# Optimization experiments

Measured on AMD Instinct MI355X. Metric: run time of the kernel, lower is better.

## Reference

```python
import jax, jax.numpy as jnp
import numpy as np

N_NODES = 50000
N_EDGES = 800000
IN_DIM = 128
HIDDEN = 128
N_GRAPHS = 512


def setup_inputs() -> dict:
    key = jax.random.key(0)
    ks = jax.random.split(key, 9)
    x = jax.random.normal(ks[0], (N_NODES, IN_DIM), dtype=jnp.float32)
    edge_index = jax.random.randint(ks[1], (2, N_EDGES), 0, N_NODES, dtype=jnp.int32)
    batch = jnp.sort(jax.random.randint(ks[2], (N_NODES,), 0, N_GRAPHS, dtype=jnp.int32))
    # GCNConv params: linear (no bias) applied before propagation, bias added after.
    s1 = 1.0 / np.sqrt(IN_DIM)
    s2 = 1.0 / np.sqrt(HIDDEN)
    W1 = jax.random.uniform(ks[3], (IN_DIM, HIDDEN), jnp.float32, -s1, s1)
    b1 = jnp.zeros((HIDDEN,), jnp.float32)
    W2 = jax.random.uniform(ks[4], (HIDDEN, HIDDEN), jnp.float32, -s2, s2)
    b2 = jnp.zeros((HIDDEN,), jnp.float32)
    Wl = jax.random.uniform(ks[5], (HIDDEN, 1), jnp.float32, -s2, s2)
    bl = jax.random.uniform(ks[6], (1,), jnp.float32, -s2, s2)
    return {"x": x, "edge_index": edge_index, "batch": batch,
            "W1": W1, "b1": b1, "W2": W2, "b2": b2, "Wl": Wl, "bl": bl}


def gcn_conv(x, W, b, src, dst):
    # PyG GCNConv: h = D^{-1/2} (A + I) D^{-1/2} (x W) + b, with self-loops.
    h = x @ W                                        # [N, H]
    deg = jnp.zeros((N_NODES,), h.dtype).at[dst].add(1.0) + 1.0  # +1 for self-loop
    dinv = jax.lax.rsqrt(deg)                        # [N]
    msg = h[src] * (dinv[src] * dinv[dst])[:, None]  # [E, H] gather + normalize
    agg = jax.ops.segment_sum(msg, dst, num_segments=N_NODES)    # scatter-add
    agg = agg + h * (dinv * dinv)[:, None]           # self-loop contribution
    return agg + b


def reference(x, edge_index, batch, W1, b1, W2, b2, Wl, bl):
    src, dst = edge_index[0], edge_index[1]
    h = jax.nn.relu(gcn_conv(x, W1, b1, src, dst))
    h = jax.nn.relu(gcn_conv(h, W2, b2, src, dst))
    # global mean pool over graphs
    sums = jax.ops.segment_sum(h, batch, num_segments=N_GRAPHS)  # [G, H]
    cnt = jax.ops.segment_sum(jnp.ones((N_NODES,), h.dtype), batch, num_segments=N_GRAPHS)
    pooled = sums / jnp.maximum(cnt, 1.0)[:, None]
    return pooled @ Wl + bl
```

## Files before the change

### kernel.cpp

```cpp
#include <hip/hip_runtime.h>
#include <hip/hip_bf16.h>

#define N_NODES 50000
#define N_EDGES 800000
#define DIM 128
#define N_GRAPHS 512
#define NBUCK ((N_NODES + 63) / 64)
#define SC_CH 2048
#define SCT_BLOCKS ((N_EDGES + SC_CH - 1) / SC_CH)
#define GEMM_BLOCKS 782

typedef unsigned int uint;
typedef unsigned short ushort;
typedef __attribute__((ext_vector_type(8))) short short8;
typedef __attribute__((ext_vector_type(4))) float f32x4;

__device__ __forceinline__ ushort f2bf(float f) {
    uint u = __float_as_uint(f);
    uint r = (u + 0x7FFF + ((u >> 16) & 1)) >> 16;
    return (ushort)r;
}
__device__ __forceinline__ uint pack2(float a, float b) {
    return (uint)f2bf(a) | ((uint)f2bf(b) << 16);
}
__device__ __forceinline__ float2 unpack2(uint v) {
    return make_float2(__uint_as_float(v << 16), __uint_as_float(v & 0xFFFF0000u));
}


__global__ __launch_bounds__(256) void k_init(const float* __restrict__ W1,
                                              const float* __restrict__ W2,
                                              uint* __restrict__ wf1,
                                              uint* __restrict__ wf2,
                                              int* __restrict__ bucketCnt) {
    int t = blockIdx.x * 256 + threadIdx.x;
    if (t < NBUCK) bucketCnt[t] = 0;
    const float* W = (t < 8192) ? W1 : W2;
    uint* dst = (t < 8192) ? wf1 : wf2;
    int r = t & 8191;
    int j2 = r & 3;
    int lane = (r >> 2) & 63;
    int tk = r >> 8;
    int kc = tk & 3, ct = tk >> 2;
    int j = j2 * 2;
    int k = kc * 32 + (lane >> 4) * 8 + j;
    int n = ct * 16 + (lane & 15);
    dst[r] = pack2(W[k * 128 + n], W[(k + 1) * 128 + n]);
}


__global__ __launch_bounds__(1024) void k_bcount(const int* __restrict__ ei,
                                                 int* __restrict__ bucketCnt, int E) {
    __shared__ int h[NBUCK];
    int tid = threadIdx.x;
    for (int t = tid; t < NBUCK; t += 1024) h[t] = 0;
    __syncthreads();
    for (int e = blockIdx.x * 1024 + tid; e < E; e += gridDim.x * 1024)
        atomicAdd(&h[ei[E + e] >> 6], 1);
    __syncthreads();
    for (int t = tid; t < NBUCK; t += 1024) {
        int c = h[t];
        if (c) atomicAdd(&bucketCnt[t], c);
    }
}


__global__ __launch_bounds__(256) void k_bscan(const int* __restrict__ bucketCnt,
                                               int* __restrict__ bucketStart,
                                               int* __restrict__ bucketCursor) {
    __shared__ int wsum4[4];
    int tid = threadIdx.x;
    int base = tid * 4;
    int v[4];
    #pragma unroll
    for (int i = 0; i < 4; ++i)
        v[i] = (base + i < NBUCK) ? bucketCnt[base + i] : 0;
    int tot = v[0] + v[1] + v[2] + v[3];
    int lane = tid & 63, w = tid >> 6;
    int sc = tot;
    #pragma unroll
    for (int off = 1; off < 64; off <<= 1) {
        int u = __shfl_up(sc, off, 64);
        if (lane >= off) sc += u;
    }
    if (lane == 63) wsum4[w] = sc;
    __syncthreads();
    int woff = 0;
    #pragma unroll
    for (int ww = 0; ww < 4; ++ww) woff += (ww < w) ? wsum4[ww] : 0;
    int run = woff + sc - tot;
    #pragma unroll
    for (int i = 0; i < 4; ++i) {
        if (base + i < NBUCK) {
            bucketStart[base + i] = run;
            bucketCursor[base + i] = run;
        }
        run += v[i];
    }
    if (tid == 255) bucketStart[NBUCK] = run;
}


template<bool BF16IN, bool SCALE>
__device__ __forceinline__ void gemm_body(int blk, const void* __restrict__ Xv,
                                          const uint* __restrict__ Wfrag,
                                          const float* __restrict__ dinv,
                                          uint* __restrict__ out, int N) {
    int wv = threadIdx.x >> 6, lane = threadIdx.x & 63;
    int strip = blk * 4 + wv;
    int row0 = strip * 16;
    if (row0 >= N) return;
    int m = lane & 15;
    int kg = lane >> 4;
    int arow = row0 + m;
    bool valid = arow < N;

    short8 af[4];
    if constexpr (!BF16IN) {
        const float* X = (const float*)Xv;
        const float* base = X + (size_t)arow * DIM + kg * 8;
        #pragma unroll
        for (int kc = 0; kc < 4; ++kc) {
            float4 a0 = make_float4(0.f, 0.f, 0.f, 0.f), a1 = a0;
            if (valid) {
                a0 = *(const float4*)(base + kc * 32);
                a1 = *(const float4*)(base + kc * 32 + 4);
            }
            short8 f;
            f[0] = (short)f2bf(a0.x); f[1] = (short)f2bf(a0.y);
            f[2] = (short)f2bf(a0.z); f[3] = (short)f2bf(a0.w);
            f[4] = (short)f2bf(a1.x); f[5] = (short)f2bf(a1.y);
            f[6] = (short)f2bf(a1.z); f[7] = (short)f2bf(a1.w);
            af[kc] = f;
        }
    } else {
        const uint* X = (const uint*)Xv;
        const uint* base = X + (size_t)arow * 64 + kg * 4;
        #pragma unroll
        for (int kc = 0; kc < 4; ++kc) {
            union { uint4 u; short8 s; } cv;
            cv.u = valid ? *(const uint4*)(base + kc * 16) : make_uint4(0, 0, 0, 0);
            af[kc] = cv.s;
        }
    }

    f32x4 acc[8];
    #pragma unroll
    for (int ct = 0; ct < 8; ++ct) acc[ct] = (f32x4){0.f, 0.f, 0.f, 0.f};

    #pragma unroll
    for (int ct = 0; ct < 8; ++ct) {
        #pragma unroll
        for (int kc = 0; kc < 4; ++kc) {
            union { uint4 u; short8 s; } bv;
            bv.u = *(const uint4*)(Wfrag + ((size_t)(ct * 4 + kc) * 64 + lane) * 4);
            acc[ct] = __builtin_amdgcn_mfma_f32_16x16x32_bf16(af[kc], bv.s, acc[ct], 0, 0, 0);
        }
    }

    ushort* ob = (ushort*)out;
    #pragma unroll
    for (int reg = 0; reg < 4; ++reg) {
        int orow = row0 + kg * 4 + reg;
        if (orow < N) {
            float di = SCALE ? dinv[orow] : 1.0f;
            size_t rb = (size_t)orow * DIM + m;
            #pragma unroll
            for (int ct = 0; ct < 8; ++ct)
                ob[rb + ct * 16] = f2bf(SCALE ? acc[ct][reg] * di : acc[ct][reg]);
        }
    }
}


__global__ __launch_bounds__(256) void k_mega1(const int* __restrict__ ei,
                                               int* __restrict__ bucketCursor,
                                               uint* __restrict__ epk,
                                               const float* __restrict__ x,
                                               const uint* __restrict__ wf1,
                                               uint* __restrict__ hs) {
    __shared__ int hc[NBUCK];
    __shared__ int hbase[NBUCK];
    if (blockIdx.x >= SCT_BLOCKS) {
        gemm_body<false, false>(blockIdx.x - SCT_BLOCKS, x, wf1, nullptr, hs, N_NODES);
        return;
    }
    int tid = threadIdx.x;
    int e0 = blockIdx.x * SC_CH;
    int e1 = min(e0 + SC_CH, N_EDGES);
    for (int t = tid; t < NBUCK; t += 256) hc[t] = 0;
    __syncthreads();
    for (int e = e0 + tid; e < e1; e += 256)
        atomicAdd(&hc[ei[N_EDGES + e] >> 6], 1);
    __syncthreads();
    for (int t = tid; t < NBUCK; t += 256) {
        int c = hc[t];
        hbase[t] = c ? atomicAdd(&bucketCursor[t], c) : 0;
        hc[t] = 0;
    }
    __syncthreads();
    for (int e = e0 + tid; e < e1; e += 256) {
        int s = ei[e], d = ei[N_EDGES + e];
        int b = d >> 6;
        int off = atomicAdd(&hc[b], 1);
        epk[hbase[b] + off] = (uint)s | ((uint)(d & 63) << 16);
    }
}


__global__ __launch_bounds__(256) void k_localcsr(const uint* __restrict__ epk,
                                                  const int* __restrict__ bucketStart,
                                                  int* __restrict__ rowStart,
                                                  float* __restrict__ dinv,
                                                  int* __restrict__ csr) {
    __shared__ int cnt[64];
    __shared__ int cur[64];
    int tid = threadIdx.x;
    int b = blockIdx.x;
    int b0 = b << 6;
    int s = bucketStart[b], e = bucketStart[b + 1];
    if (tid < 64) cnt[tid] = 0;
    __syncthreads();
    for (int i = s + tid; i < e; i += 256)
        atomicAdd(&cnt[(epk[i] >> 16) & 63], 1);
    __syncthreads();
    if (tid < 64) {
        int c = cnt[tid];
        int sc = c;
        #pragma unroll
        for (int off = 1; off < 64; off <<= 1) {
            int u = __shfl_up(sc, off, 64);
            if (tid >= off) sc += u;
        }
        int excl = sc - c;
        int node = b0 + tid;
        if (node < N_NODES) {
            rowStart[node] = s + excl;
            dinv[node] = rsqrtf((float)c + 1.0f);
        }
        cur[tid] = s + excl;
    }
    if (tid == 0 && b == NBUCK - 1) rowStart[N_NODES] = e;
    __syncthreads();
    for (int i = s + tid; i < e; i += 256) {
        uint p = epk[i];
        int pos = atomicAdd(&cur[(p >> 16) & 63], 1);
        csr[pos] = (int)(p & 0xFFFFu);
    }
}


__global__ __launch_bounds__(256) void k_lin2(const uint* __restrict__ Xb,
                                              const uint* __restrict__ Wfrag,
                                              const float* __restrict__ dinv,
                                              uint* __restrict__ out, int N) {
    gemm_body<true, true>(blockIdx.x, Xb, Wfrag, dinv, out, N);
}


template<bool FUSE_HEAD, bool SCALE_SRC>
__global__ __launch_bounds__(256) void k_aggregate(const uint* __restrict__ HS,
                                                   const int* __restrict__ rowStart,
                                                   const int* __restrict__ csr,
                                                   const float* __restrict__ dinv,
                                                   const float* __restrict__ bias,
                                                   const float* __restrict__ Wl,
                                                   uint* __restrict__ outRow,
                                                   float* __restrict__ outY, int n) {
    int wv = threadIdx.x >> 6, lane = threadIdx.x & 63;
    int nid = blockIdx.x * 4 + wv;
    if (nid >= n) return;
    float di = dinv[nid];
    float2 acc = unpack2(HS[(size_t)nid * 64 + lane]);
    if constexpr (SCALE_SRC) { acc.x *= di; acc.y *= di; }
    int beg = rowStart[nid], end = rowStart[nid + 1];
    int e = beg;
    for (; e + 7 < end; e += 8) {
        int s0 = csr[e],     s1 = csr[e + 1], s2 = csr[e + 2], s3 = csr[e + 3];
        int s4 = csr[e + 4], s5 = csr[e + 5], s6 = csr[e + 6], s7 = csr[e + 7];
        float2 f0 = unpack2(HS[(size_t)s0 * 64 + lane]);
        float2 f1 = unpack2(HS[(size_t)s1 * 64 + lane]);
        float2 f2 = unpack2(HS[(size_t)s2 * 64 + lane]);
        float2 f3 = unpack2(HS[(size_t)s3 * 64 + lane]);
        float2 f4 = unpack2(HS[(size_t)s4 * 64 + lane]);
        float2 f5 = unpack2(HS[(size_t)s5 * 64 + lane]);
        float2 f6 = unpack2(HS[(size_t)s6 * 64 + lane]);
        float2 f7 = unpack2(HS[(size_t)s7 * 64 + lane]);
        if constexpr (SCALE_SRC) {
            float d0 = dinv[s0], d1 = dinv[s1], d2 = dinv[s2], d3 = dinv[s3];
            float d4 = dinv[s4], d5 = dinv[s5], d6 = dinv[s6], d7 = dinv[s7];
            acc.x += ((f0.x * d0 + f1.x * d1) + (f2.x * d2 + f3.x * d3))
                   + ((f4.x * d4 + f5.x * d5) + (f6.x * d6 + f7.x * d7));
            acc.y += ((f0.y * d0 + f1.y * d1) + (f2.y * d2 + f3.y * d3))
                   + ((f4.y * d4 + f5.y * d5) + (f6.y * d6 + f7.y * d7));
        } else {
            acc.x += ((f0.x + f1.x) + (f2.x + f3.x)) + ((f4.x + f5.x) + (f6.x + f7.x));
            acc.y += ((f0.y + f1.y) + (f2.y + f3.y)) + ((f4.y + f5.y) + (f6.y + f7.y));
        }
    }
    if (e + 3 < end) {
        int s0 = csr[e], s1 = csr[e + 1], s2 = csr[e + 2], s3 = csr[e + 3];
        float2 f0 = unpack2(HS[(size_t)s0 * 64 + lane]);
        float2 f1 = unpack2(HS[(size_t)s1 * 64 + lane]);
        float2 f2 = unpack2(HS[(size_t)s2 * 64 + lane]);
        float2 f3 = unpack2(HS[(size_t)s3 * 64 + lane]);
        if constexpr (SCALE_SRC) {
            float d0 = dinv[s0], d1 = dinv[s1], d2 = dinv[s2], d3 = dinv[s3];
            acc.x += (f0.x * d0 + f1.x * d1) + (f2.x * d2 + f3.x * d3);
            acc.y += (f0.y * d0 + f1.y * d1) + (f2.y * d2 + f3.y * d3);
        } else {
            acc.x += (f0.x + f1.x) + (f2.x + f3.x);
            acc.y += (f0.y + f1.y) + (f2.y + f3.y);
        }
        e += 4;
    }
    if (e + 1 < end) {
        int s0 = csr[e], s1 = csr[e + 1];
        float2 f0 = unpack2(HS[(size_t)s0 * 64 + lane]);
        float2 f1 = unpack2(HS[(size_t)s1 * 64 + lane]);
        if constexpr (SCALE_SRC) {
            float d0 = dinv[s0], d1 = dinv[s1];
            acc.x += f0.x * d0 + f1.x * d1;
            acc.y += f0.y * d0 + f1.y * d1;
        } else {
            acc.x += f0.x + f1.x;
            acc.y += f0.y + f1.y;
        }
        e += 2;
    }
    if (e < end) {
        int s0 = csr[e];
        float2 f0 = unpack2(HS[(size_t)s0 * 64 + lane]);
        if constexpr (SCALE_SRC) {
            float d0 = dinv[s0];
            acc.x += f0.x * d0;
            acc.y += f0.y * d0;
        } else {
            acc.x += f0.x;
            acc.y += f0.y;
        }
    }
    int c = lane * 2;
    float ox = fmaxf(acc.x * di + bias[c], 0.f);
    float oy = fmaxf(acc.y * di + bias[c + 1], 0.f);
    if constexpr (!FUSE_HEAD) {
        outRow[(size_t)nid * 64 + lane] = pack2(ox, oy);
    } else {
        float part = ox * Wl[c] + oy * Wl[c + 1];
        #pragma unroll
        for (int off = 32; off > 0; off >>= 1) part += __shfl_down(part, off, 64);
        if (lane == 0) outY[nid] = part;
    }
}


__global__ __launch_bounds__(64) void k_pool_y(const float* __restrict__ y,
                                               const int* __restrict__ batch,
                                               const float* __restrict__ bl,
                                               float* __restrict__ out, int n) {
    int g = blockIdx.x;
    int lane = threadIdx.x;
    int lo = 0, hi = n;
    while (lo < hi) { int mid = (lo + hi) >> 1; if (batch[mid] < g) lo = mid + 1; else hi = mid; }
    int s = lo;
    hi = n;
    while (lo < hi) { int mid = (lo + hi) >> 1; if (batch[mid] < g + 1) lo = mid + 1; else hi = mid; }
    int e = lo;

    float sum = 0.f;
    for (int i = s + lane; i < e; i += 64) sum += y[i];
    #pragma unroll
    for (int off = 32; off > 0; off >>= 1) sum += __shfl_down(sum, off, 64);
    if (lane == 0) out[g] = sum / fmaxf((float)(e - s), 1.0f) + bl[0];
}


extern "C" void kernel_launch(void* const* d_in, const int* in_sizes, int n_in,
                              void* d_out, int out_size, void* d_ws, size_t ws_size,
                              hipStream_t stream) {
    const float* x  = (const float*)d_in[0];
    const int*   ei = (const int*)d_in[1];
    const int*   batch = (const int*)d_in[2];
    const float* W1 = (const float*)d_in[3];
    const float* b1 = (const float*)d_in[4];
    const float* W2 = (const float*)d_in[5];
    const float* b2 = (const float*)d_in[6];
    const float* Wl = (const float*)d_in[7];
    const float* bl = (const float*)d_in[8];
    float* out = (float*)d_out;

    uint* hs  = (uint*)d_ws;
    uint* h2b = hs + (size_t)N_NODES * 64;
    float* dinv = (float*)(h2b + (size_t)N_NODES * 64);
    float* ynode = dinv + N_NODES;
    int* rowStart = (int*)(ynode + N_NODES);
    int* bucketCnt = rowStart + N_NODES + 4;
    int* bucketStart = bucketCnt + 788;
    int* bucketCursor = bucketStart + 788;
    int* csr = bucketCursor + 788;
    uint* epk = (uint*)(csr + N_EDGES);
    uint* wf1 = epk + N_EDGES;
    uint* wf2 = wf1 + 8192;

    k_init<<<64, 256, 0, stream>>>(W1, W2, wf1, wf2, bucketCnt);

    k_bcount<<<64, 1024, 0, stream>>>(ei, bucketCnt, N_EDGES);

    k_bscan<<<1, 256, 0, stream>>>(bucketCnt, bucketStart, bucketCursor);

    k_mega1<<<SCT_BLOCKS + GEMM_BLOCKS, 256, 0, stream>>>(ei, bucketCursor, epk, x, wf1, hs);

    k_localcsr<<<NBUCK, 256, 0, stream>>>(epk, bucketStart, rowStart, dinv, csr);

    int aggGrid = (N_NODES + 3) / 4;

    k_aggregate<false, true><<<aggGrid, 256, 0, stream>>>(
        hs, rowStart, csr, dinv, b1, Wl, h2b, ynode, N_NODES);

    k_lin2<<<GEMM_BLOCKS, 256, 0, stream>>>(h2b, wf2, dinv, hs, N_NODES);

    k_aggregate<true, false><<<aggGrid, 256, 0, stream>>>(
        hs, rowStart, csr, dinv, b2, Wl, h2b, ynode, N_NODES);

    k_pool_y<<<N_GRAPHS, 64, 0, stream>>>(ynode, batch, bl, out, N_NODES);
}
```

Baseline: 142.3 us.

## Fuse CSR build stages into one persistent kernel with grid barriers

Replaces the separate bucket-count, scan, scatter and local-CSR kernels with a single kernel. 512 CSR blocks synchronise through a software grid barrier (atomic counter plus generation flag), while extra blocks in the same launch run the first GEMM. The aim is to remove several kernel launch gaps and the per-stage drain. The barrier only works if all 512 CSR blocks are resident at once, so there is a deadlock risk, and the spin-waiting blocks compete with the GEMM blocks for compute units.

```diff
diff --git a/kernel.cpp b/kernel.cpp
--- a/kernel.cpp
+++ b/kernel.cpp
@@ -6,8 +6,8 @@
 #define DIM 128
 #define N_GRAPHS 512
 #define NBUCK ((N_NODES + 63) / 64)
-#define SC_CH 2048
-#define SCT_BLOCKS ((N_EDGES + SC_CH - 1) / SC_CH)
+#define CSRB 512
+#define EPB ((N_EDGES + CSRB - 1) / CSRB)
 #define GEMM_BLOCKS 782
 
 typedef unsigned int uint;
@@ -32,9 +32,11 @@
                                               const float* __restrict__ W2,
                                               uint* __restrict__ wf1,
                                               uint* __restrict__ wf2,
-                                              int* __restrict__ bucketCnt) {
+                                              int* __restrict__ bucketCnt,
+                                              int* __restrict__ bar) {
     int t = blockIdx.x * 256 + threadIdx.x;
     if (t < NBUCK) bucketCnt[t] = 0;
+    if (t >= NBUCK && t < NBUCK + 2) bar[t - NBUCK] = 0;
     const float* W = (t < 8192) ? W1 : W2;
     uint* dst = (t < 8192) ? wf1 : wf2;
     int r = t & 8191;
@@ -49,55 +51,22 @@
 }
 
 
-__global__ __launch_bounds__(1024) void k_bcount(const int* __restrict__ ei,
-                                                 int* __restrict__ bucketCnt, int E) {
-    __shared__ int h[NBUCK];
-    int tid = threadIdx.x;
-    for (int t = tid; t < NBUCK; t += 1024) h[t] = 0;
+__device__ __forceinline__ void gbar(int* barCnt, int* barGen, int phase) {
     __syncthreads();
-    for (int e = blockIdx.x * 1024 + tid; e < E; e += gridDim.x * 1024)
-        atomicAdd(&h[ei[E + e] >> 6], 1);
+    if (threadIdx.x == 0) {
+        __threadfence();
+        if (atomicAdd(barCnt, 1) == CSRB - 1) {
+            atomicExch(barCnt, 0);
+            __threadfence();
+            atomicAdd(barGen, 1);
+        } else {
+            while (atomicAdd(barGen, 0) <= phase) {
+                __builtin_amdgcn_s_sleep(2);
+            }
+        }
+        __threadfence();
+    }
     __syncthreads();
-    for (int t = tid; t < NBUCK; t += 1024) {
-        int c = h[t];
-        if (c) atomicAdd(&bucketCnt[t], c);
-    }
-}
-
-
-__global__ __launch_bounds__(256) void k_bscan(const int* __restrict__ bucketCnt,
-                                               int* __restrict__ bucketStart,
-                                               int* __restrict__ bucketCursor) {
-    __shared__ int wsum4[4];
-    int tid = threadIdx.x;
-    int base = tid * 4;
-    int v[4];
-    #pragma unroll
-    for (int i = 0; i < 4; ++i)
-        v[i] = (base + i < NBUCK) ? bucketCnt[base + i] : 0;
-    int tot = v[0] + v[1] + v[2] + v[3];
-    int lane = tid & 63, w = tid >> 6;
-    int sc = tot;
-    #pragma unroll
-    for (int off = 1; off < 64; off <<= 1) {
-        int u = __shfl_up(sc, off, 64);
-        if (lane >= off) sc += u;
-    }
-    if (lane == 63) wsum4[w] = sc;
-    __syncthreads();
-    int woff = 0;
-    #pragma unroll
-    for (int ww = 0; ww < 4; ++ww) woff += (ww < w) ? wsum4[ww] : 0;
-    int run = woff + sc - tot;
-    #pragma unroll
-    for (int i = 0; i < 4; ++i) {
-        if (base + i < NBUCK) {
-            bucketStart[base + i] = run;
-            bucketCursor[base + i] = run;
-        }
-        run += v[i];
-    }
-    if (tid == 255) bucketStart[NBUCK] = run;
 }
 
 
@@ -173,21 +142,33 @@
 }
 
 
-__global__ __launch_bounds__(256) void k_mega1(const int* __restrict__ ei,
+__global__ __launch_bounds__(256) void k_build(const int* __restrict__ ei,
+                                               int* __restrict__ bucketCnt,
+                                               int* __restrict__ bucketStart,
                                                int* __restrict__ bucketCursor,
                                                uint* __restrict__ epk,
+                                               int* __restrict__ rowStart,
+                                               float* __restrict__ dinv,
+                                               int* __restrict__ csr,
+                                               int* __restrict__ bar,
                                                const float* __restrict__ x,
                                                const uint* __restrict__ wf1,
                                                uint* __restrict__ hs) {
+    if (blockIdx.x >= CSRB) {
+        gemm_body<false, false>(blockIdx.x - CSRB, x, wf1, nullptr, hs, N_NODES);
+        return;
+    }
     __shared__ int hc[NBUCK];
     __shared__ int hbase[NBUCK];
-    if (blockIdx.x >= SCT_BLOCKS) {
-        gemm_body<false, false>(blockIdx.x - SCT_BLOCKS, x, wf1, nullptr, hs, N_NODES);
-        return;
-    }
+    __shared__ int wsum4[4];
+    __shared__ int cnt[64];
+    __shared__ int cur[64];
+    int cb = blockIdx.x;
     int tid = threadIdx.x;
-    int e0 = blockIdx.x * SC_CH;
-    int e1 = min(e0 + SC_CH, N_EDGES);
+    int* barCnt = bar;
+    int* barGen = bar + 1;
+    int e0 = cb * EPB, e1 = min(e0 + EPB, N_EDGES);
+
     for (int t = tid; t < NBUCK; t += 256) hc[t] = 0;
     __syncthreads();
     for (int e = e0 + tid; e < e1; e += 256)
@@ -195,6 +176,44 @@
     __syncthreads();
     for (int t = tid; t < NBUCK; t += 256) {
         int c = hc[t];
+        if (c) atomicAdd(&bucketCnt[t], c);
+    }
+    gbar(barCnt, barGen, 0);
+
+    if (cb == 0) {
+        int base = tid * 4;
+        int v[4];
+        #pragma unroll
+        for (int i = 0; i < 4; ++i)
+            v[i] = (base + i < NBUCK) ? bucketCnt[base + i] : 0;
+        int tot = v[0] + v[1] + v[2] + v[3];
+        int lane = tid & 63, w = tid >> 6;
+        int sc = tot;
+        #pragma unroll
+        for (int off = 1; off < 64; off <<= 1) {
+            int u = __shfl_up(sc, off, 64);
+            if (lane >= off) sc += u;
+        }
+        if (lane == 63) wsum4[w] = sc;
+        __syncthreads();
+        int woff = 0;
+        #pragma unroll
+        for (int ww = 0; ww < 4; ++ww) woff += (ww < w) ? wsum4[ww] : 0;
+        int run = woff + sc - tot;
+        #pragma unroll
+        for (int i = 0; i < 4; ++i) {
+            if (base + i < NBUCK) {
+                bucketStart[base + i] = run;
+                bucketCursor[base + i] = run;
+            }
+            run += v[i];
+        }
+        if (tid == 255) bucketStart[NBUCK] = run;
+    }
+    gbar(barCnt, barGen, 1);
+
+    for (int t = tid; t < NBUCK; t += 256) {
+        int c = hc[t];
         hbase[t] = c ? atomicAdd(&bucketCursor[t], c) : 0;
         hc[t] = 0;
     }
@@ -205,47 +224,40 @@
         int off = atomicAdd(&hc[b], 1);
         epk[hbase[b] + off] = (uint)s | ((uint)(d & 63) << 16);
     }
-}
-
-
-__global__ __launch_bounds__(256) void k_localcsr(const uint* __restrict__ epk,
-                                                  const int* __restrict__ bucketStart,
-                                                  int* __restrict__ rowStart,
-                                                  float* __restrict__ dinv,
-                                                  int* __restrict__ csr) {
-    __shared__ int cnt[64];
-    __shared__ int cur[64];
-    int tid = threadIdx.x;
-    int b = blockIdx.x;
-    int b0 = b << 6;
-    int s = bucketStart[b], e = bucketStart[b + 1];
-    if (tid < 64) cnt[tid] = 0;
-    __syncthreads();
-    for (int i = s + tid; i < e; i += 256)
-        atomicAdd(&cnt[(epk[i] >> 16) & 63], 1);
-    __syncthreads();
-    if (tid < 64) {
-        int c = cnt[tid];
-        int sc = c;
-        #pragma unroll
-        for (int off = 1; off < 64; off <<= 1) {
-            int u = __shfl_up(sc, off, 64);
-            if (tid >= off) sc += u;
-        }
-        int excl = sc - c;
-        int node = b0 + tid;
-        if (node < N_NODES) {
-            rowStart[node] = s + excl;
-            dinv[node] = rsqrtf((float)c + 1.0f);
-        }
-        cur[tid] = s + excl;
-    }
-    if (tid == 0 && b == NBUCK - 1) rowStart[N_NODES] = e;
-    __syncthreads();
-    for (int i = s + tid; i < e; i += 256) {
-        uint p = epk[i];
-        int pos = atomicAdd(&cur[(p >> 16) & 63], 1);
-        csr[pos] = (int)(p & 0xFFFFu);
+    gbar(barCnt, barGen, 2);
+
+    for (int b = cb; b < NBUCK; b += CSRB) {
+        int b0 = b << 6;
+        int s = bucketStart[b], e = bucketStart[b + 1];
+        if (tid < 64) cnt[tid] = 0;
+        __syncthreads();
+        for (int i = s + tid; i < e; i += 256)
+            atomicAdd(&cnt[(epk[i] >> 16) & 63], 1);
+        __syncthreads();
+        if (tid < 64) {
+            int c = cnt[tid];
+            int sc = c;
+            #pragma unroll
+            for (int off = 1; off < 64; off <<= 1) {
+                int u = __shfl_up(sc, off, 64);
+                if (tid >= off) sc += u;
+            }
+            int excl = sc - c;
+            int node = b0 + tid;
+            if (node < N_NODES) {
+                rowStart[node] = s + excl;
+                dinv[node] = rsqrtf((float)c + 1.0f);
+            }
+            cur[tid] = s + excl;
+        }
+        if (tid == 0 && b == NBUCK - 1) rowStart[N_NODES] = e;
+        __syncthreads();
+        for (int i = s + tid; i < e; i += 256) {
+            uint p = epk[i];
+            int pos = atomicAdd(&cur[(p >> 16) & 63], 1);
+            csr[pos] = (int)(p & 0xFFFFu);
+        }
+        __syncthreads();
     }
 }
 
@@ -397,20 +409,17 @@
     int* bucketCnt = rowStart + N_NODES + 4;
     int* bucketStart = bucketCnt + 788;
     int* bucketCursor = bucketStart + 788;
-    int* csr = bucketCursor + 788;
+    int* bar = bucketCursor + 788;
+    int* csr = bar + 4;
     uint* epk = (uint*)(csr + N_EDGES);
     uint* wf1 = epk + N_EDGES;
     uint* wf2 = wf1 + 8192;
 
-    k_init<<<64, 256, 0, stream>>>(W1, W2, wf1, wf2, bucketCnt);
-
-    k_bcount<<<64, 1024, 0, stream>>>(ei, bucketCnt, N_EDGES);
-
-    k_bscan<<<1, 256, 0, stream>>>(bucketCnt, bucketStart, bucketCursor);
-
-    k_mega1<<<SCT_BLOCKS + GEMM_BLOCKS, 256, 0, stream>>>(ei, bucketCursor, epk, x, wf1, hs);
-
-    k_localcsr<<<NBUCK, 256, 0, stream>>>(epk, bucketStart, rowStart, dinv, csr);
+    k_init<<<64, 256, 0, stream>>>(W1, W2, wf1, wf2, bucketCnt, bar);
+
+    k_build<<<CSRB + GEMM_BLOCKS, 256, 0, stream>>>(
+        ei, bucketCnt, bucketStart, bucketCursor, epk, rowStart, dinv, csr, bar,
+        x, wf1, hs);
 
     int aggGrid = (N_NODES + 3) / 4;
 
```

After: 297.1 us. 2.09x slower.
